# Kernel optimization log

Hardware: AMD Instinct MI355X
Metric: run time of the kernel (lower is better)

Reference implementation:

```python
import jax, jax.numpy as jnp
import numpy as np

EPS = 1e-5
B, S, E = 4, 2048, 2048
H, DH = 16, 128
F = 8192


def rmsnorm(x, gamma):
    # Keras LayerNormalization(rms_scaling=True): x * rsqrt(mean(x^2)+eps) * gamma
    return x * jax.lax.rsqrt(jnp.mean(jnp.square(x), axis=-1, keepdims=True) + EPS) * gamma


def rope(x, positions, head_dim):
    # Rotary embedding applied per head_dim-sized chunk of the embedding axis
    b, s, e = x.shape
    x = x.reshape(b, s, e // head_dim, head_dim)
    half = head_dim // 2
    inv_freq = 1.0 / (10000.0 ** (jnp.arange(half, dtype=x.dtype) / half))  # [half]
    ang = positions.astype(x.dtype)[:, None] * inv_freq  # [S, half]
    cos = jnp.concatenate([jnp.cos(ang), jnp.cos(ang)], axis=-1)[None, :, None, :]
    sin = jnp.concatenate([jnp.sin(ang), jnp.sin(ang)], axis=-1)[None, :, None, :]
    x1, x2 = x[..., :half], x[..., half:]
    rot = jnp.concatenate([-x2, x1], axis=-1)
    return (x * cos + rot * sin).reshape(b, s, e)


def setup_inputs() -> dict:
    key = jax.random.key(0)
    ks = jax.random.split(key, 12)
    std = 0.02
    return {
        "inputs": jax.random.normal(ks[0], (B, S, E), dtype=jnp.float32),
        "gamma_attn": jnp.ones((E,), dtype=jnp.float32),
        "gamma_ffn": jnp.ones((E,), dtype=jnp.float32),
        "wq": jax.random.normal(ks[1], (E, H, DH), dtype=jnp.float32) * std,
        "wk": jax.random.normal(ks[2], (E, H, DH), dtype=jnp.float32) * std,
        "wv": jax.random.normal(ks[3], (E, H, DH), dtype=jnp.float32) * std,
        "wo": jax.random.normal(ks[4], (H, DH, E), dtype=jnp.float32) * std,
        "w_gate": jax.random.normal(ks[5], (E, F), dtype=jnp.float32) * std,
        "w_lin": jax.random.normal(ks[6], (E, F), dtype=jnp.float32) * std,
        "w_out": jax.random.normal(ks[7], (F, E), dtype=jnp.float32) * std,
        "positions": jnp.arange(S, dtype=jnp.int32),
        "cache": jnp.zeros((1,), dtype=jnp.int32),
        "mask": jnp.ones((B, S), dtype=bool),
    }


def reference(inputs, gamma_attn, gamma_ffn, wq, wk, wv, wo, w_gate, w_lin, w_out, positions, cache, mask):
    x = inputs
    # --- attention sub-block ---
    y = rmsnorm(x, gamma_attn)
    y = rope(y, positions, DH)
    q = jnp.einsum("bse,ehd->bshd", y, wq)
    k = jnp.einsum("bse,ehd->bshd", y, wk)
    v = jnp.einsum("bse,ehd->bshd", y, wv)
    scores = jnp.einsum("bqhd,bkhd->bhqk", q, k) / jnp.sqrt(jnp.asarray(DH, q.dtype))
    causal = jnp.tril(jnp.ones((S, S), dtype=bool))
    scores = jnp.where(causal[None, None], scores, jnp.asarray(-1e9, scores.dtype))
    probs = jax.nn.softmax(scores, axis=-1)
    attn = jnp.einsum("bhqk,bkhd->bqhd", probs, v)
    y = jnp.einsum("bqhd,hde->bqe", attn, wo)
    x = y + x
    # --- FFN sub-block (gelu-gated) ---
    y = rmsnorm(x, gamma_ffn)
    y = jnp.einsum("bse,ef->bsf", jax.nn.gelu(y @ w_gate, approximate=False) * (y @ w_lin), jnp.eye(F, dtype=y.dtype)) if False else (jax.nn.gelu(y @ w_gate, approximate=False) * (y @ w_lin)) @ w_out
    return y + x
```

## Files before the change

kernel.cpp:

```cpp
#include <hip/hip_runtime.h>
#include <cstdint>
#include <cstddef>

#define B_ 4
#define S_ 2048
#define E_ 2048
#define H_ 16
#define DH_ 128
#define F_ 8192
#define NTOK (B_*S_)
#define QKVN (3*E_)

typedef __attribute__((ext_vector_type(4))) float f32x4;
typedef __attribute__((ext_vector_type(8))) __bf16 bf16x8;
typedef __attribute__((ext_vector_type(8))) short s16x8;
typedef __attribute__((ext_vector_type(4))) short s16x4;

using gas_ptr = const __attribute__((address_space(1))) void*;
using las_ptr = __attribute__((address_space(3))) void*;

__device__ __forceinline__ short f2bf(float f) {
  union { float f; uint32_t u; } v{f};
  uint32_t r = v.u + 0x7FFFu + ((v.u >> 16) & 1u);
  return (short)(r >> 16);
}
__device__ __forceinline__ float bf2f(short s) {
  union { uint32_t u; float f; } v;
  v.u = ((uint32_t)(uint16_t)s) << 16;
  return v.f;
}

__global__ __launch_bounds__(256) void k_rms_rope(const float* __restrict__ x,
                                                  const float* __restrict__ gamma,
                                                  const int* __restrict__ pos,
                                                  short* __restrict__ y) {
  const int row = blockIdx.x;
  const int s = row & (S_ - 1);
  const int t = threadIdx.x;
  const int head = t >> 4;
  const int j0 = (t & 15) << 2;
  const float* xr = x + (size_t)row * E_;
  const int c1 = head * DH_ + j0;
  const int c2 = c1 + 64;
  f32x4 x1 = *(const f32x4*)(xr + c1);
  f32x4 x2 = *(const f32x4*)(xr + c2);
  float ss = x1[0]*x1[0]+x1[1]*x1[1]+x1[2]*x1[2]+x1[3]*x1[3]
           + x2[0]*x2[0]+x2[1]*x2[1]+x2[2]*x2[2]+x2[3]*x2[3];
  #pragma unroll
  for (int off = 32; off >= 1; off >>= 1) ss += __shfl_xor(ss, off, 64);
  __shared__ float red[4];
  __shared__ float rsh;
  if ((t & 63) == 0) red[t >> 6] = ss;
  __syncthreads();
  if (t == 0) rsh = rsqrtf((red[0]+red[1]+red[2]+red[3]) * (1.0f / E_) + 1e-5f);
  __syncthreads();
  const float r = rsh;
  f32x4 g1 = *(const f32x4*)(gamma + c1);
  f32x4 g2 = *(const f32x4*)(gamma + c2);
  const float p = (float)pos[s];
  s16x4 o1, o2;
  #pragma unroll
  for (int jj = 0; jj < 4; ++jj) {
    float fi = exp2f((float)(j0 + jj) * (-13.287712379549449f / 64.0f));
    float ang = p * fi;
    float sn, cs;
    sincosf(ang, &sn, &cs);
    float a = x1[jj] * r * g1[jj];
    float b = x2[jj] * r * g2[jj];
    o1[jj] = f2bf(a * cs - b * sn);
    o2[jj] = f2bf(b * cs + a * sn);
  }
  *(s16x4*)(y + (size_t)row * E_ + c1) = o1;
  *(s16x4*)(y + (size_t)row * E_ + c2) = o2;
}

__global__ __launch_bounds__(256) void k_rms(const float* __restrict__ x,
                                             const float* __restrict__ gamma,
                                             short* __restrict__ y) {
  const int row = blockIdx.x;
  const int t = threadIdx.x;
  const int c = t << 3;
  const float* xr = x + (size_t)row * E_;
  f32x4 a = *(const f32x4*)(xr + c);
  f32x4 b = *(const f32x4*)(xr + c + 4);
  float ss = a[0]*a[0]+a[1]*a[1]+a[2]*a[2]+a[3]*a[3]
           + b[0]*b[0]+b[1]*b[1]+b[2]*b[2]+b[3]*b[3];
  #pragma unroll
  for (int off = 32; off >= 1; off >>= 1) ss += __shfl_xor(ss, off, 64);
  __shared__ float red[4];
  __shared__ float rsh;
  if ((t & 63) == 0) red[t >> 6] = ss;
  __syncthreads();
  if (t == 0) rsh = rsqrtf((red[0]+red[1]+red[2]+red[3]) * (1.0f / E_) + 1e-5f);
  __syncthreads();
  const float r = rsh;
  f32x4 ga = *(const f32x4*)(gamma + c);
  f32x4 gb = *(const f32x4*)(gamma + c + 4);
  s16x8 o;
  #pragma unroll
  for (int jj = 0; jj < 4; ++jj) {
    o[jj]   = f2bf(a[jj] * r * ga[jj]);
    o[4+jj] = f2bf(b[jj] * r * gb[jj]);
  }
  *(s16x8*)(y + (size_t)row * E_ + c) = o;
}

__global__ __launch_bounds__(256) void k_transpose_f32_bf16(const float* __restrict__ src,
                                                            short* __restrict__ dst,
                                                            int R, int C) {
  __shared__ float tile[32][33];
  const int c0 = blockIdx.x << 5, r0 = blockIdx.y << 5;
  const int tx = threadIdx.x & 31, ty = threadIdx.x >> 5;
  #pragma unroll
  for (int j = 0; j < 32; j += 8)
    tile[ty + j][tx] = src[(size_t)(r0 + ty + j) * C + c0 + tx];
  __syncthreads();
  #pragma unroll
  for (int j = 0; j < 32; j += 8)
    dst[(size_t)(c0 + ty + j) * R + r0 + tx] = f2bf(tile[tx][ty + j]);
}

__global__ __launch_bounds__(256) void k_transpose_v(const short* __restrict__ qkv,
                                                     short* __restrict__ vt) {
  __shared__ short tile[32][33];
  const int bh = blockIdx.z;
  const short* src = qkv + (size_t)(bh >> 4) * S_ * QKVN + 2 * E_ + (bh & 15) * DH_;
  short* dst = vt + (size_t)bh * DH_ * S_;
  const int s0 = blockIdx.x << 5, d0 = blockIdx.y << 5;
  const int tx = threadIdx.x & 31, ty = threadIdx.x >> 5;
  #pragma unroll
  for (int j = 0; j < 32; j += 8)
    tile[ty + j][tx] = src[(size_t)(s0 + ty + j) * QKVN + d0 + tx];
  __syncthreads();
  #pragma unroll
  for (int j = 0; j < 32; j += 8)
    dst[(size_t)(d0 + ty + j) * S_ + s0 + tx] = tile[tx][ty + j];
}

template<int EPI>
__global__ __launch_bounds__(512, 2) void k_gemm(const short* __restrict__ A,
                                                 const short* __restrict__ Bt,
                                                 void* Cv, const void* aux,
                                                 int M, int N, int K) {
  __shared__ __align__(16) short As[5 * 256 * 32];
  __shared__ __align__(16) short Bs[4 * 256 * 32];
  const int tiles_n = gridDim.x;
  const int nwg = tiles_n * (int)gridDim.y;
  int bid = (int)blockIdx.y * tiles_n + (int)blockIdx.x;
  if ((nwg & 7) == 0) bid = (bid & 7) * (nwg >> 3) + (bid >> 3);
  const int m_tile = bid / tiles_n, n_tile = bid - m_tile * tiles_n;
  const int m0 = m_tile << 8, n0 = n_tile << 8;

  const int tid = threadIdx.x;
  const int wave = tid >> 6, lane = tid & 63;
  const int ll = lane & 15, lh = lane >> 4;
  const int wm = wave >> 2, wn = wave & 3;

  const int sr0 = tid >> 2;
  const int g = (tid & 3) ^ ((sr0 & 3) ^ ((sr0 >> 2) & 3));
  const short* Ag0 = A  + (size_t)(m0 + sr0) * K + g * 8;
  const short* Bg0 = Bt + (size_t)(n0 + sr0) * K + g * 8;
  const size_t rstep = (size_t)128 * K;
  const int wuB = wave << 9;

  const int NKT = K >> 6;
  const int HMAX = NKT << 2;

  auto STAGE = [&](int h) {
    if (h > HMAX - 1) h = HMAX - 1;
    const int sidx = h >> 1;
    const int koff = ((h >> 2) << 6) + (((h >> 1) & 1) << 5);
    if ((h & 1) == 0) {
      const int sl = (sidx % 5) << 13;
      __builtin_amdgcn_global_load_lds((gas_ptr)(Ag0 + koff),
                                       (las_ptr)(As + sl + wuB), 16, 0, 0);
      __builtin_amdgcn_global_load_lds((gas_ptr)(Ag0 + koff + rstep),
                                       (las_ptr)(As + sl + 4096 + wuB), 16, 0, 0);
    } else {
      const int sl = (sidx & 3) << 13;
      __builtin_amdgcn_global_load_lds((gas_ptr)(Bg0 + koff),
                                       (las_ptr)(Bs + sl + wuB), 16, 0, 0);
      __builtin_amdgcn_global_load_lds((gas_ptr)(Bg0 + koff + rstep),
                                       (las_ptr)(Bs + sl + 4096 + wuB), 16, 0, 0);
    }
  };

  const f32x4 fz = {0.f, 0.f, 0.f, 0.f};
  f32x4 acc[8][4];
  #pragma unroll
  for (int i = 0; i < 8; ++i)
    #pragma unroll
    for (int j = 0; j < 4; ++j) acc[i][j] = fz;

  const int sA = (ll & 3) ^ ((ll >> 2) & 3);
  const int cOff = (lh ^ sA) << 3;
  const int rdA = (((wm << 7) + ll) << 5) + cOff;
  const int rdB = (((wn << 6) + ll) << 5) + cOff;

  #pragma unroll
  for (int h = 0; h < 7; ++h) STAGE(h);
  asm volatile("s_waitcnt vmcnt(6)" ::: "memory");
  __builtin_amdgcn_s_barrier();

  for (int kt = 0; kt < NKT; ++kt) {
    const int hb = (kt << 2) + 7;
    const int slA0 = ((2 * kt) % 5) << 13;
    const int slA1 = ((2 * kt + 1) % 5) << 13;
    const int slB0 = ((2 * kt) & 3) << 13;
    const int slB1 = slB0 + (1 << 13);
    bf16x8 bA[4], bB[4];

    #pragma unroll
    for (int nf = 0; nf < 4; ++nf) bB[nf] = *(const bf16x8*)&Bs[slB0 + rdB + nf * 512];
    #pragma unroll
    for (int mf = 0; mf < 4; ++mf) bA[mf] = *(const bf16x8*)&As[slA0 + rdA + mf * 512];
    STAGE(hb);
    __builtin_amdgcn_s_barrier();
    asm volatile("s_waitcnt lgkmcnt(0)" ::: "memory");
    __builtin_amdgcn_s_setprio(1);
    #pragma unroll
    for (int mf = 0; mf < 4; ++mf)
      #pragma unroll
      for (int nf = 0; nf < 4; ++nf)
        acc[mf][nf] = __builtin_amdgcn_mfma_f32_16x16x32_bf16(bA[mf], bB[nf], acc[mf][nf], 0, 0, 0);
    __builtin_amdgcn_s_setprio(0);
    __builtin_amdgcn_s_barrier();

    #pragma unroll
    for (int mf = 0; mf < 4; ++mf) bA[mf] = *(const bf16x8*)&As[slA0 + rdA + 2048 + mf * 512];
    STAGE(hb + 1);
    __builtin_amdgcn_s_barrier();
    asm volatile("s_waitcnt lgkmcnt(0)" ::: "memory");
    __builtin_amdgcn_s_setprio(1);
    #pragma unroll
    for (int mf = 0; mf < 4; ++mf)
      #pragma unroll
      for (int nf = 0; nf < 4; ++nf)
        acc[4 + mf][nf] = __builtin_amdgcn_mfma_f32_16x16x32_bf16(bA[mf], bB[nf], acc[4 + mf][nf], 0, 0, 0);
    __builtin_amdgcn_s_setprio(0);
    __builtin_amdgcn_s_barrier();

    #pragma unroll
    for (int nf = 0; nf < 4; ++nf) bB[nf] = *(const bf16x8*)&Bs[slB1 + rdB + nf * 512];
    #pragma unroll
    for (int mf = 0; mf < 4; ++mf) bA[mf] = *(const bf16x8*)&As[slA1 + rdA + mf * 512];
    STAGE(hb + 2);
    __builtin_amdgcn_s_barrier();
    asm volatile("s_waitcnt lgkmcnt(0)" ::: "memory");
    __builtin_amdgcn_s_setprio(1);
    #pragma unroll
    for (int mf = 0; mf < 4; ++mf)
      #pragma unroll
      for (int nf = 0; nf < 4; ++nf)
        acc[mf][nf] = __builtin_amdgcn_mfma_f32_16x16x32_bf16(bA[mf], bB[nf], acc[mf][nf], 0, 0, 0);
    __builtin_amdgcn_s_setprio(0);
    __builtin_amdgcn_s_barrier();

    #pragma unroll
    for (int mf = 0; mf < 4; ++mf) bA[mf] = *(const bf16x8*)&As[slA1 + rdA + 2048 + mf * 512];
    STAGE(hb + 3);
    __builtin_amdgcn_s_barrier();
    asm volatile("s_waitcnt lgkmcnt(0)" ::: "memory");
    __builtin_amdgcn_s_setprio(1);
    #pragma unroll
    for (int mf = 0; mf < 4; ++mf)
      #pragma unroll
      for (int nf = 0; nf < 4; ++nf)
        acc[4 + mf][nf] = __builtin_amdgcn_mfma_f32_16x16x32_bf16(bA[mf], bB[nf], acc[4 + mf][nf], 0, 0, 0);
    __builtin_amdgcn_s_setprio(0);
    asm volatile("s_waitcnt vmcnt(6)" ::: "memory");
    __builtin_amdgcn_s_barrier();
  }

  #pragma unroll
  for (int mf = 0; mf < 8; ++mf) {
    const int row = m0 + (wm << 7) + (mf << 4) + (lh << 2);
    #pragma unroll
    for (int nf = 0; nf < 4; ++nf) {
      const int col = n0 + (wn << 6) + (nf << 4) + ll;
      #pragma unroll
      for (int rg = 0; rg < 4; ++rg) {
        const float c = acc[mf][nf][rg];
        const size_t idx = (size_t)(row + rg) * N + col;
        if constexpr (EPI == 0) {
          ((short*)Cv)[idx] = f2bf(c);
        } else if constexpr (EPI == 1) {
          ((float*)Cv)[idx] = c + ((const float*)aux)[idx];
        } else if constexpr (EPI == 2) {
          float gl = 0.5f * c * (1.0f + erff(c * 0.70710678118654752f));
          ((short*)Cv)[idx] = f2bf(gl);
        } else {
          float gl = bf2f(((short*)Cv)[idx]);
          ((short*)Cv)[idx] = f2bf(c * gl);
        }
      }
    }
  }
}

#define CEXP 0.12752682475470602f
__global__ __launch_bounds__(256, 2) void k_flash(const short* __restrict__ qkv,
                                                  const short* __restrict__ vt,
                                                  short* __restrict__ attn) {
  __shared__ short Kt[64][136];
  __shared__ short VtT[128][72];
  __shared__ short Pt[4][32][72];
  const int qt = blockIdx.x, bh = blockIdx.y;
  const int b = bh >> 4, h = bh & 15;
  const int q0 = qt << 7;
  const int tid = threadIdx.x, wave = tid >> 6, lane = tid & 63;
  const int ll = lane & 15, lh = lane >> 4;
  const short* qbase = qkv + (size_t)b * S_ * QKVN + h * DH_;
  const short* kbase = qbase + E_;
  const short* vbase = vt + (size_t)bh * DH_ * S_;

  bf16x8 qf[2][4];
  #pragma unroll
  for (int mt = 0; mt < 2; ++mt) {
    const short* qr = qbase + (size_t)(q0 + wave * 32 + mt * 16 + ll) * QKVN;
    #pragma unroll
    for (int kc = 0; kc < 4; ++kc) qf[mt][kc] = *(const bf16x8*)(qr + kc * 32 + lh * 8);
  }

  const f32x4 fzero = {0.f, 0.f, 0.f, 0.f};
  float m_i[2][4], l_i[2][4];
  f32x4 oacc[2][8];
  #pragma unroll
  for (int mt = 0; mt < 2; ++mt) {
    #pragma unroll
    for (int rg = 0; rg < 4; ++rg) { m_i[mt][rg] = -1e30f; l_i[mt][rg] = 0.f; }
    #pragma unroll
    for (int n8 = 0; n8 < 8; ++n8) oacc[mt][n8] = fzero;
  }

  const int nkt = (q0 + 128) >> 6;
  for (int kt = 0; kt < nkt; ++kt) {
    const int k0 = kt << 6;
    __syncthreads();
    #pragma unroll
    for (int p = 0; p < 4; ++p) {
      int idx = p * 256 + tid;
      int r = idx >> 4, c0 = (idx & 15) << 3;
      *(s16x8*)&Kt[r][c0] = *(const s16x8*)(kbase + (size_t)(k0 + r) * QKVN + c0);
      int dh = idx >> 3, kk = (idx & 7) << 3;
      *(s16x8*)&VtT[dh][kk] = *(const s16x8*)(vbase + (size_t)dh * S_ + k0 + kk);
    }
    __syncthreads();

    f32x4 sc[2][4];
    #pragma unroll
    for (int mt = 0; mt < 2; ++mt)
      #pragma unroll
      for (int nt = 0; nt < 4; ++nt) sc[mt][nt] = fzero;
    #pragma unroll
    for (int kc = 0; kc < 4; ++kc) {
      bf16x8 kb[4];
      #pragma unroll
      for (int nt = 0; nt < 4; ++nt)
        kb[nt] = *(const bf16x8*)&Kt[nt * 16 + ll][kc * 32 + lh * 8];
      #pragma unroll
      for (int mt = 0; mt < 2; ++mt)
        #pragma unroll
        for (int nt = 0; nt < 4; ++nt)
          sc[mt][nt] = __builtin_amdgcn_mfma_f32_16x16x32_bf16(qf[mt][kc], kb[nt], sc[mt][nt], 0, 0, 0);
    }

    if (k0 + 63 > q0) {
      #pragma unroll
      for (int mt = 0; mt < 2; ++mt)
        #pragma unroll
        for (int nt = 0; nt < 4; ++nt)
          #pragma unroll
          for (int rg = 0; rg < 4; ++rg) {
            int kidx = k0 + nt * 16 + ll;
            int qidx = q0 + wave * 32 + mt * 16 + lh * 4 + rg;
            if (kidx > qidx) sc[mt][nt][rg] = -1e30f;
          }
    }

    #pragma unroll
    for (int mt = 0; mt < 2; ++mt)
      #pragma unroll
      for (int rg = 0; rg < 4; ++rg) {
        float mx = fmaxf(fmaxf(sc[mt][0][rg], sc[mt][1][rg]),
                         fmaxf(sc[mt][2][rg], sc[mt][3][rg]));
        #pragma unroll
        for (int off = 1; off < 16; off <<= 1) mx = fmaxf(mx, __shfl_xor(mx, off, 64));
        float mn = fmaxf(m_i[mt][rg], mx);
        float al = exp2f((m_i[mt][rg] - mn) * CEXP);
        m_i[mt][rg] = mn;
        float rsum = 0.f;
        #pragma unroll
        for (int nt = 0; nt < 4; ++nt) {
          float pv = exp2f((sc[mt][nt][rg] - mn) * CEXP);
          sc[mt][nt][rg] = pv;
          rsum += pv;
        }
        #pragma unroll
        for (int off = 1; off < 16; off <<= 1) rsum += __shfl_xor(rsum, off, 64);
        l_i[mt][rg] = l_i[mt][rg] * al + rsum;
        #pragma unroll
        for (int n8 = 0; n8 < 8; ++n8) oacc[mt][n8][rg] *= al;
      }

    #pragma unroll
    for (int mt = 0; mt < 2; ++mt)
      #pragma unroll
      for (int nt = 0; nt < 4; ++nt)
        #pragma unroll
        for (int rg = 0; rg < 4; ++rg)
          Pt[wave][mt * 16 + lh * 4 + rg][nt * 16 + ll] = f2bf(sc[mt][nt][rg]);

    #pragma unroll
    for (int kc2 = 0; kc2 < 2; ++kc2) {
      bf16x8 pa[2];
      #pragma unroll
      for (int mt = 0; mt < 2; ++mt)
        pa[mt] = *(const bf16x8*)&Pt[wave][mt * 16 + ll][kc2 * 32 + lh * 8];
      #pragma unroll
      for (int n8 = 0; n8 < 8; ++n8) {
        bf16x8 vb = *(const bf16x8*)&VtT[n8 * 16 + ll][kc2 * 32 + lh * 8];
        #pragma unroll
        for (int mt = 0; mt < 2; ++mt)
          oacc[mt][n8] = __builtin_amdgcn_mfma_f32_16x16x32_bf16(pa[mt], vb, oacc[mt][n8], 0, 0, 0);
      }
    }
  }

  short* ab = attn + (size_t)(b * S_) * E_ + h * DH_;
  #pragma unroll
  for (int mt = 0; mt < 2; ++mt) {
    const int row = q0 + wave * 32 + mt * 16 + lh * 4;
    #pragma unroll
    for (int n8 = 0; n8 < 8; ++n8) {
      const int col = n8 * 16 + ll;
      #pragma unroll
      for (int rg = 0; rg < 4; ++rg)
        ab[(size_t)(row + rg) * E_ + col] = f2bf(oacc[mt][n8][rg] / l_i[mt][rg]);
    }
  }
}

extern "C" void kernel_launch(void* const* d_in, const int* in_sizes, int n_in,
                              void* d_out, int out_size, void* d_ws, size_t ws_size,
                              hipStream_t stream) {
  (void)in_sizes; (void)n_in; (void)out_size; (void)ws_size;
  const float* x      = (const float*)d_in[0];
  const float* g_attn = (const float*)d_in[1];
  const float* g_ffn  = (const float*)d_in[2];
  const float* wq     = (const float*)d_in[3];
  const float* wk     = (const float*)d_in[4];
  const float* wv     = (const float*)d_in[5];
  const float* wo     = (const float*)d_in[6];
  const float* wg     = (const float*)d_in[7];
  const float* wl     = (const float*)d_in[8];
  const float* wout   = (const float*)d_in[9];
  const int*   pos    = (const int*)d_in[10];

  char* wsb = (char*)d_ws;
  short* W    = (short*)wsb;
  short* BIG  = (short*)(wsb + (size_t)33554432);
  short* ACT  = (short*)(wsb + (size_t)33554432 + 134217728);

  short* QKV  = BIG;
  short* VT   = BIG + (size_t)NTOK * QKVN;
  short* Hb   = BIG;
  short* Y1   = ACT;
  short* ATTN = ACT;
  short* Y2   = ACT;
  float* X2   = (float*)d_out;

  const dim3 blk(256);
  const dim3 gblk(512);

  k_transpose_f32_bf16<<<dim3(64, 64), blk, 0, stream>>>(wq, W,                   2048, 2048);
  k_transpose_f32_bf16<<<dim3(64, 64), blk, 0, stream>>>(wk, W + 2048 * 2048,     2048, 2048);
  k_transpose_f32_bf16<<<dim3(64, 64), blk, 0, stream>>>(wv, W + 2 * 2048 * 2048, 2048, 2048);

  k_rms_rope<<<NTOK, blk, 0, stream>>>(x, g_attn, pos, Y1);
  k_gemm<0><<<dim3(QKVN / 256, NTOK / 256), gblk, 0, stream>>>(Y1, W, QKV, nullptr, NTOK, QKVN, E_);
  k_transpose_v<<<dim3(S_ / 32, DH_ / 32, B_ * H_), blk, 0, stream>>>(QKV, VT);
  k_flash<<<dim3(S_ / 128, B_ * H_), blk, 0, stream>>>(QKV, VT, ATTN);

  k_transpose_f32_bf16<<<dim3(64, 64), blk, 0, stream>>>(wo, W, 2048, 2048);
  k_gemm<1><<<dim3(E_ / 256, NTOK / 256), gblk, 0, stream>>>(ATTN, W, X2, x, NTOK, E_, E_);

  k_rms<<<NTOK, blk, 0, stream>>>(X2, g_ffn, Y2);

  k_transpose_f32_bf16<<<dim3(256, 64), blk, 0, stream>>>(wg, W, 2048, 8192);
  k_gemm<2><<<dim3(F_ / 256, NTOK / 256), gblk, 0, stream>>>(Y2, W, Hb, nullptr, NTOK, F_, E_);
  k_transpose_f32_bf16<<<dim3(256, 64), blk, 0, stream>>>(wl, W, 2048, 8192);
  k_gemm<3><<<dim3(F_ / 256, NTOK / 256), gblk, 0, stream>>>(Y2, W, Hb, nullptr, NTOK, F_, E_);
  k_transpose_f32_bf16<<<dim3(64, 256), blk, 0, stream>>>(wout, W, 8192, 2048);
  k_gemm<1><<<dim3(E_ / 256, NTOK / 256), gblk, 0, stream>>>(Hb, W, d_out, X2, NTOK, E_, F_);
}
```

Before: 2.112 ms.

## Restructure GEMM LDS staging into 128x64 half-tiles with shallower prefetch

The GEMM's shared-memory layout changes from 256x32 k-slices to 128-row by 64-wide half-tiles, with a new XOR swizzle for the 8-element chunks. The single interleaved STAGE helper is replaced by separate A and B half-tile loaders, and the prefetch schedule now issues one half-tile per sub-step. Each wave reads its own half of A and B, so every global load fetches a full 64-wide K row segment. This aims for more contiguous global loads and fewer outstanding loads (vmcnt 2 instead of 6). The cost is a shallower prefetch depth and the risk of stalls or bank conflicts from the new swizzle.

```diff
diff --git a/kernel.cpp b/kernel.cpp
--- a/kernel.cpp
+++ b/kernel.cpp
@@ -142,8 +142,8 @@
                                                  const short* __restrict__ Bt,
                                                  void* Cv, const void* aux,
                                                  int M, int N, int K) {
-  __shared__ __align__(16) short As[5 * 256 * 32];
-  __shared__ __align__(16) short Bs[4 * 256 * 32];
+  __shared__ __align__(16) short As[5 * 128 * 64];
+  __shared__ __align__(16) short Bs[4 * 128 * 64];
   const int tiles_n = gridDim.x;
   const int nwg = tiles_n * (int)gridDim.y;
   int bid = (int)blockIdx.y * tiles_n + (int)blockIdx.x;
@@ -156,33 +156,31 @@
   const int ll = lane & 15, lh = lane >> 4;
   const int wm = wave >> 2, wn = wave & 3;
 
-  const int sr0 = tid >> 2;
-  const int g = (tid & 3) ^ ((sr0 & 3) ^ ((sr0 >> 2) & 3));
-  const short* Ag0 = A  + (size_t)(m0 + sr0) * K + g * 8;
-  const short* Bg0 = Bt + (size_t)(n0 + sr0) * K + g * 8;
-  const size_t rstep = (size_t)128 * K;
+  const int sr = tid >> 3;
+  const int chk = (tid & 7) ^ (((tid >> 5) & 1) << 1);
+  const short* Ag0 = A  + (size_t)(m0 + sr) * K + chk * 8;
+  const short* Bg0 = Bt + (size_t)(n0 + sr) * K + chk * 8;
   const int wuB = wave << 9;
 
   const int NKT = K >> 6;
-  const int HMAX = NKT << 2;
-
-  auto STAGE = [&](int h) {
-    if (h > HMAX - 1) h = HMAX - 1;
-    const int sidx = h >> 1;
-    const int koff = ((h >> 2) << 6) + (((h >> 1) & 1) << 5);
-    if ((h & 1) == 0) {
-      const int sl = (sidx % 5) << 13;
-      __builtin_amdgcn_global_load_lds((gas_ptr)(Ag0 + koff),
-                                       (las_ptr)(As + sl + wuB), 16, 0, 0);
-      __builtin_amdgcn_global_load_lds((gas_ptr)(Ag0 + koff + rstep),
-                                       (las_ptr)(As + sl + 4096 + wuB), 16, 0, 0);
-    } else {
-      const int sl = (sidx & 3) << 13;
-      __builtin_amdgcn_global_load_lds((gas_ptr)(Bg0 + koff),
-                                       (las_ptr)(Bs + sl + wuB), 16, 0, 0);
-      __builtin_amdgcn_global_load_lds((gas_ptr)(Bg0 + koff + rstep),
-                                       (las_ptr)(Bs + sl + 4096 + wuB), 16, 0, 0);
-    }
+
+  auto STAGE_A = [&](int t2, int half) {
+    if (t2 > NKT - 1) t2 = NKT - 1;
+    const int sl = ((2 * t2 + half) % 5) << 13;
+    const short* src = Ag0 + (size_t)(half * 128) * K + t2 * 64;
+    __builtin_amdgcn_global_load_lds((gas_ptr)src,
+                                     (las_ptr)(As + sl + wuB), 16, 0, 0);
+    __builtin_amdgcn_global_load_lds((gas_ptr)(src + (size_t)64 * K),
+                                     (las_ptr)(As + sl + 4096 + wuB), 16, 0, 0);
+  };
+  auto STAGE_B = [&](int t2, int half) {
+    if (t2 > NKT - 1) t2 = NKT - 1;
+    const int sl = ((2 * t2 + half) & 3) << 13;
+    const short* src = Bg0 + (size_t)(half * 128) * K + t2 * 64;
+    __builtin_amdgcn_global_load_lds((gas_ptr)src,
+                                     (las_ptr)(Bs + sl + wuB), 16, 0, 0);
+    __builtin_amdgcn_global_load_lds((gas_ptr)(src + (size_t)64 * K),
+                                     (las_ptr)(Bs + sl + 4096 + wuB), 16, 0, 0);
   };
 
   const f32x4 fz = {0.f, 0.f, 0.f, 0.f};
@@ -192,29 +190,26 @@
     #pragma unroll
     for (int j = 0; j < 4; ++j) acc[i][j] = fz;
 
-  const int sA = (ll & 3) ^ ((ll >> 2) & 3);
-  const int cOff = (lh ^ sA) << 3;
-  const int rdA = (((wm << 7) + ll) << 5) + cOff;
-  const int rdB = (((wn << 6) + ll) << 5) + cOff;
-
-  #pragma unroll
-  for (int h = 0; h < 7; ++h) STAGE(h);
-  asm volatile("s_waitcnt vmcnt(6)" ::: "memory");
+  const int swsh = ((ll >> 2) & 1) << 4;
+  const int c0s = (lh << 3) ^ swsh;
+  const int c1s = (32 + (lh << 3)) ^ swsh;
+  const int rAb = (ll << 6);
+  const int rBb = ((wn & 1) << 12) + (ll << 6);
+
+  STAGE_A(0, 0); STAGE_A(0, 1); STAGE_B(0, 0); STAGE_B(0, 1); STAGE_A(1, 0);
+  asm volatile("s_waitcnt vmcnt(2)" ::: "memory");
   __builtin_amdgcn_s_barrier();
 
   for (int kt = 0; kt < NKT; ++kt) {
-    const int hb = (kt << 2) + 7;
-    const int slA0 = ((2 * kt) % 5) << 13;
-    const int slA1 = ((2 * kt + 1) % 5) << 13;
-    const int slB0 = ((2 * kt) & 3) << 13;
-    const int slB1 = slB0 + (1 << 13);
+    const int slA = ((2 * kt + wm) % 5) << 13;
+    const int slB = ((2 * kt + (wn >> 1)) & 3) << 13;
     bf16x8 bA[4], bB[4];
 
     #pragma unroll
-    for (int nf = 0; nf < 4; ++nf) bB[nf] = *(const bf16x8*)&Bs[slB0 + rdB + nf * 512];
-    #pragma unroll
-    for (int mf = 0; mf < 4; ++mf) bA[mf] = *(const bf16x8*)&As[slA0 + rdA + mf * 512];
-    STAGE(hb);
+    for (int nf = 0; nf < 4; ++nf) bB[nf] = *(const bf16x8*)&Bs[slB + rBb + nf * 1024 + c0s];
+    #pragma unroll
+    for (int mf = 0; mf < 4; ++mf) bA[mf] = *(const bf16x8*)&As[slA + rAb + mf * 1024 + c0s];
+    STAGE_A(kt + 1, 1);
     __builtin_amdgcn_s_barrier();
     asm volatile("s_waitcnt lgkmcnt(0)" ::: "memory");
     __builtin_amdgcn_s_setprio(1);
@@ -227,8 +222,8 @@
     __builtin_amdgcn_s_barrier();
 
     #pragma unroll
-    for (int mf = 0; mf < 4; ++mf) bA[mf] = *(const bf16x8*)&As[slA0 + rdA + 2048 + mf * 512];
-    STAGE(hb + 1);
+    for (int mf = 0; mf < 4; ++mf) bA[mf] = *(const bf16x8*)&As[slA + rAb + (mf + 4) * 1024 + c0s];
+    STAGE_B(kt + 1, 0);
     __builtin_amdgcn_s_barrier();
     asm volatile("s_waitcnt lgkmcnt(0)" ::: "memory");
     __builtin_amdgcn_s_setprio(1);
@@ -241,10 +236,10 @@
     __builtin_amdgcn_s_barrier();
 
     #pragma unroll
-    for (int nf = 0; nf < 4; ++nf) bB[nf] = *(const bf16x8*)&Bs[slB1 + rdB + nf * 512];
-    #pragma unroll
-    for (int mf = 0; mf < 4; ++mf) bA[mf] = *(const bf16x8*)&As[slA1 + rdA + mf * 512];
-    STAGE(hb + 2);
+    for (int nf = 0; nf < 4; ++nf) bB[nf] = *(const bf16x8*)&Bs[slB + rBb + nf * 1024 + c1s];
+    #pragma unroll
+    for (int mf = 0; mf < 4; ++mf) bA[mf] = *(const bf16x8*)&As[slA + rAb + mf * 1024 + c1s];
+    STAGE_B(kt + 1, 1);
     __builtin_amdgcn_s_barrier();
     asm volatile("s_waitcnt lgkmcnt(0)" ::: "memory");
     __builtin_amdgcn_s_setprio(1);
@@ -257,8 +252,8 @@
     __builtin_amdgcn_s_barrier();
 
     #pragma unroll
-    for (int mf = 0; mf < 4; ++mf) bA[mf] = *(const bf16x8*)&As[slA1 + rdA + 2048 + mf * 512];
-    STAGE(hb + 3);
+    for (int mf = 0; mf < 4; ++mf) bA[mf] = *(const bf16x8*)&As[slA + rAb + (mf + 4) * 1024 + c1s];
+    STAGE_A(kt + 2, 0);
     __builtin_amdgcn_s_barrier();
     asm volatile("s_waitcnt lgkmcnt(0)" ::: "memory");
     __builtin_amdgcn_s_setprio(1);
@@ -268,7 +263,7 @@
       for (int nf = 0; nf < 4; ++nf)
         acc[4 + mf][nf] = __builtin_amdgcn_mfma_f32_16x16x32_bf16(bA[mf], bB[nf], acc[4 + mf][nf], 0, 0, 0);
     __builtin_amdgcn_s_setprio(0);
-    asm volatile("s_waitcnt vmcnt(6)" ::: "memory");
+    asm volatile("s_waitcnt vmcnt(2)" ::: "memory");
     __builtin_amdgcn_s_barrier();
   }
 
```

After: 2.032 ms. 1.04x faster.
